# Kernel optimization log

Measured on AMD Instinct MI355X. Metric: run time of the kernel, lower is better.

The kernel has to match this reference:

```python
import jax, jax.numpy as jnp
import numpy as np

B, S, D, H = 4, 2048, 1024, 16
DK = D // H


def setup_inputs() -> dict:
    key = jax.random.key(0)
    ks = jax.random.split(key, 11)
    std = 1.0 / np.sqrt(D)
    mk = lambda k: jax.random.uniform(k, (D, D), jnp.float32, -std, std)
    mb = lambda k: jax.random.uniform(k, (D,), jnp.float32, -std, std)
    return {
        "query": jax.random.normal(ks[0], (B, S, D), jnp.float32),
        "key": jax.random.normal(ks[1], (B, S, D), jnp.float32),
        "value": jax.random.normal(ks[2], (B, S, D), jnp.float32),
        "Wq": mk(ks[3]), "bq": mb(ks[4]),
        "Wk": mk(ks[5]), "bk": mb(ks[6]),
        "Wv": mk(ks[7]), "bv": mb(ks[8]),
        "Wo": mk(ks[9]), "bo": mb(ks[10]),
    }


def reference(query, key, value, Wq, bq, Wk, bk, Wv, bv, Wo, bo):
    # Linear projections (torch Linear: x @ W.T + b)
    Q = query @ Wq.T + bq   # [B,S,D]
    K = key @ Wk.T + bk
    V = value @ Wv.T + bv
    # split heads -> [B,H,S,DK]
    Q = Q.reshape(B, S, H, DK).transpose(0, 2, 1, 3)
    K = K.reshape(B, S, H, DK).transpose(0, 2, 1, 3)
    V = V.reshape(B, S, H, DK).transpose(0, 2, 1, 3)
    scale = 1.0 / jnp.sqrt(jnp.asarray(DK, Q.dtype))
    scores = jnp.einsum("bhqd,bhkd->bhqk", Q, K) * scale  # [B,H,S,S]
    attn = jax.nn.softmax(scores, axis=-1)
    out = jnp.einsum("bhqk,bhkd->bhqd", attn, V)          # [B,H,S,DK]
    out = out.transpose(0, 2, 1, 3).reshape(B, S, D)       # [B,S,D]
    return out @ Wo.T + bo
```

## Files before the change

### kernel.cpp

```cpp
#include <hip/hip_runtime.h>
#include <hip/hip_bf16.h>
#include <stdint.h>


using f32x4  = __attribute__((ext_vector_type(4))) float;
using f32x16 = __attribute__((ext_vector_type(16))) float;
using s16x8  = __attribute__((ext_vector_type(8))) short;
using u16x8  = __attribute__((ext_vector_type(8))) unsigned short;
using u16x4  = __attribute__((ext_vector_type(4))) unsigned short;

#define MFMA16(a, b, c) __builtin_amdgcn_mfma_f32_16x16x32_bf16((a), (b), (c), 0, 0, 0)
#define MFMA32(a, b, c) __builtin_amdgcn_mfma_f32_32x32x16_bf16((a), (b), (c), 0, 0, 0)

#define GLL16(gptr, lptr)                                                      \
  __builtin_amdgcn_global_load_lds(                                            \
      (const __attribute__((address_space(1))) void*)(gptr),                   \
      (__attribute__((address_space(3))) void*)(lptr), 16, 0, 0)

__device__ __forceinline__ unsigned short f2bf(float f) {
  union { __hip_bfloat16 h; unsigned short u; } cv;
  cv.h = __float2bfloat16(f);
  return cv.u;
}

__device__ __forceinline__ unsigned int pkbf(float a, float b) {
  return (unsigned int)f2bf(a) | ((unsigned int)f2bf(b) << 16);
}

__device__ __forceinline__ s16x8 pack8(const float4& a, const float4& b) {
  union { u16x8 u; s16x8 s; } cv;
  cv.u[0] = f2bf(a.x); cv.u[1] = f2bf(a.y); cv.u[2] = f2bf(a.z); cv.u[3] = f2bf(a.w);
  cv.u[4] = f2bf(b.x); cv.u[5] = f2bf(b.y); cv.u[6] = f2bf(b.z); cv.u[7] = f2bf(b.w);
  return cv.s;
}

__global__ __launch_bounds__(256) void cast_w_kernel(
    const float* __restrict__ wq, const float* __restrict__ wk,
    const float* __restrict__ wv, const float* __restrict__ wo,
    unsigned short* __restrict__ dst) {
  int i = blockIdx.x * 256 + threadIdx.x;
  int m = i >> 18;
  int off = i & 0x3FFFF;
  const float* src = (m == 0) ? wq : (m == 1) ? wk : (m == 2) ? wv : wo;
  float4 v = reinterpret_cast<const float4*>(src)[off];
  u16x4 o;
  o[0] = f2bf(v.x); o[1] = f2bf(v.y); o[2] = f2bf(v.z); o[3] = f2bf(v.w);
  *reinterpret_cast<u16x4*>(dst + (size_t)i * 4) = o;
}

__global__ __launch_bounds__(256) void gemm_qkv_kernel(
    const float* __restrict__ xq, const float* __restrict__ xk, const float* __restrict__ xv,
    const unsigned short* __restrict__ wbf,
    const float* __restrict__ bq, const float* __restrict__ bk, const float* __restrict__ bv,
    unsigned short* __restrict__ Qh, unsigned short* __restrict__ Kh,
    unsigned short* __restrict__ Vh) {
  const int z = blockIdx.z;
  const float* X = (z == 0) ? xq : (z == 1) ? xk : xv;
  const float* bias = (z == 0) ? bq : (z == 1) ? bk : bv;
  const unsigned short* W = wbf + (size_t)z * 1048576;
  unsigned short* dst = (z == 0) ? Qh : (z == 1) ? Kh : Vh;
  const float qscale = (z == 0) ? 0.18033688011112042f : 1.0f;

  __shared__ __align__(16) float Af[128 * 32];
  __shared__ __align__(16) unsigned short Bs[128 * 32];

  const int t = threadIdx.x;
  const int lane = t & 63, w = t >> 6;
  const int g = lane >> 4, c = lane & 15;
  const int wm = (w >> 1) * 64, wn = (w & 1) * 64;
  const int n0 = (blockIdx.y & 7) * 128;
  const int m0 = (blockIdx.x * 8 + (blockIdx.y >> 3)) * 128;

  f32x4 acc[4][4];
#pragma unroll
  for (int i = 0; i < 4; i++)
#pragma unroll
    for (int j = 0; j < 4; j++) acc[i][j] = (f32x4)0.0f;

  const int ar = lane >> 3;
  const int acs = (lane & 7) ^ ar;
  const int br_ = lane >> 2;
  const int bcs = (lane & 3) ^ (br_ & 3);

  for (int k0 = 0; k0 < 1024; k0 += 32) {
    __syncthreads();
#pragma unroll
    for (int i = 0; i < 4; i++) {
      int ii = w * 4 + i;
      const float* gsrc = X + (size_t)(m0 + ii * 8 + ar) * 1024 + k0 + acs * 4;
      GLL16(gsrc, &Af[ii * 256]);
    }
#pragma unroll
    for (int i = 0; i < 2; i++) {
      int ii = w * 2 + i;
      const unsigned short* gsrc = W + (size_t)(n0 + ii * 16 + br_) * 1024 + k0 + bcs * 8;
      GLL16(gsrc, &Bs[ii * 512]);
    }
    __syncthreads();

    s16x8 af[4], bfr[4];
#pragma unroll
    for (int mt = 0; mt < 4; mt++) {
      int r = wm + mt * 16 + c;
      int x = r & 7;
      const float* rowp = &Af[r * 32];
      float4 f0 = *reinterpret_cast<const float4*>(rowp + (((g * 2) ^ x) << 2));
      float4 f1 = *reinterpret_cast<const float4*>(rowp + (((g * 2 + 1) ^ x) << 2));
      af[mt] = pack8(f0, f1);
    }
#pragma unroll
    for (int nt = 0; nt < 4; nt++) {
      int r = wn + nt * 16 + c;
      bfr[nt] = *reinterpret_cast<const s16x8*>(&Bs[r * 32 + ((g ^ (r & 3)) << 3)]);
    }
#pragma unroll
    for (int mt = 0; mt < 4; mt++)
#pragma unroll
      for (int nt = 0; nt < 4; nt++)
        acc[mt][nt] = MFMA16(af[mt], bfr[nt], acc[mt][nt]);
  }

#pragma unroll
  for (int mt = 0; mt < 4; mt++)
#pragma unroll
    for (int nt = 0; nt < 4; nt++) {
      int n = n0 + wn + nt * 16 + c;
      float bb = bias[n];
      int h = n >> 6, dk = n & 63;
#pragma unroll
      for (int r = 0; r < 4; r++) {
        int m = m0 + wm + mt * 16 + g * 4 + r;
        int b = m >> 11, s = m & 2047;
        dst[(((size_t)b * 16 + h) * 2048 + s) * 64 + dk] =
            f2bf((acc[mt][nt][r] + bb) * qscale);
      }
    }
}

__global__ __launch_bounds__(256) void gemm_out_kernel(
    const unsigned short* __restrict__ AO, const unsigned short* __restrict__ Wo,
    const float* __restrict__ bo, float* __restrict__ out) {
  __shared__ __align__(16) unsigned short Asm_[128 * 32];
  __shared__ __align__(16) unsigned short Bsm_[128 * 32];

  const int t = threadIdx.x;
  const int lane = t & 63, w = t >> 6;
  const int g = lane >> 4, c = lane & 15;
  const int wm = (w >> 1) * 64, wn = (w & 1) * 64;
  const int n0 = (blockIdx.y & 7) * 128;
  const int m0 = (blockIdx.x * 8 + (blockIdx.y >> 3)) * 128;

  f32x4 acc[4][4];
#pragma unroll
  for (int i = 0; i < 4; i++)
#pragma unroll
    for (int j = 0; j < 4; j++) acc[i][j] = (f32x4)0.0f;

  const int br_ = lane >> 2;
  const int bcs = (lane & 3) ^ (br_ & 3);

  for (int k0 = 0; k0 < 1024; k0 += 32) {
    __syncthreads();
#pragma unroll
    for (int i = 0; i < 2; i++) {
      int ii = w * 2 + i;
      const unsigned short* ga = AO + (size_t)(m0 + ii * 16 + br_) * 1024 + k0 + bcs * 8;
      GLL16(ga, &Asm_[ii * 512]);
      const unsigned short* gb = Wo + (size_t)(n0 + ii * 16 + br_) * 1024 + k0 + bcs * 8;
      GLL16(gb, &Bsm_[ii * 512]);
    }
    __syncthreads();

    s16x8 af[4], bfr[4];
#pragma unroll
    for (int mt = 0; mt < 4; mt++) {
      int r = wm + mt * 16 + c;
      af[mt] = *reinterpret_cast<const s16x8*>(&Asm_[r * 32 + ((g ^ (r & 3)) << 3)]);
    }
#pragma unroll
    for (int nt = 0; nt < 4; nt++) {
      int r = wn + nt * 16 + c;
      bfr[nt] = *reinterpret_cast<const s16x8*>(&Bsm_[r * 32 + ((g ^ (r & 3)) << 3)]);
    }
#pragma unroll
    for (int mt = 0; mt < 4; mt++)
#pragma unroll
      for (int nt = 0; nt < 4; nt++)
        acc[mt][nt] = MFMA16(af[mt], bfr[nt], acc[mt][nt]);
  }

#pragma unroll
  for (int mt = 0; mt < 4; mt++)
#pragma unroll
    for (int nt = 0; nt < 4; nt++) {
      int n = n0 + wn + nt * 16 + c;
      float bb = bo[n];
#pragma unroll
      for (int r = 0; r < 4; r++) {
        int m = m0 + wm + mt * 16 + g * 4 + r;
        out[(size_t)m * 1024 + n] = acc[mt][nt][r] + bb;
      }
    }
}

__global__ __launch_bounds__(512) void attn_kernel(
    const unsigned short* __restrict__ Qh, const unsigned short* __restrict__ Kh,
    const unsigned short* __restrict__ Vh, unsigned short* __restrict__ AO) {
  const int bh = blockIdx.x * 8 + (blockIdx.y >> 3);
  const int b = bh >> 4, h = bh & 15;
  const int q0 = (blockIdx.y & 7) * 256;
  const int t = threadIdx.x, lane = t & 63, w = t >> 6;
  const int lo = lane & 31, hi = lane >> 5;

  __shared__ __align__(16) unsigned short Ks[2][64 * 64];
  __shared__ __align__(16) unsigned short Vt[2][64 * 64];

  const size_t kvbase = (size_t)bh * 2048 * 64;

  s16x8 qb[4];
  {
    const unsigned short* qp = Qh + kvbase + (size_t)(q0 + w * 32 + lo) * 64;
#pragma unroll
    for (int ks = 0; ks < 4; ks++)
      qb[ks] = *reinterpret_cast<const s16x8*>(qp + ks * 16 + hi * 8);
  }

  f32x16 oacc[2];
  oacc[0] = (f32x16)0.0f; oacc[1] = (f32x16)0.0f;
  float lsum = 0.0f;

  const int skrow = t >> 3, sks = t & 7;
  const int kgc = sks ^ (skrow & 7);
  const int vkrow = t >> 3, vd0 = (t & 7) * 8;

  uint4 kk, vv;
  kk = *reinterpret_cast<const uint4*>(Kh + kvbase + (size_t)skrow * 64 + kgc * 8);
  vv = *reinterpret_cast<const uint4*>(Vh + kvbase + (size_t)vkrow * 64 + vd0);
  *reinterpret_cast<uint4*>(&Ks[0][(size_t)t * 8]) = kk;
  {
    const unsigned short* vs = reinterpret_cast<const unsigned short*>(&vv);
#pragma unroll
    for (int j = 0; j < 8; j++)
      Vt[0][(vd0 + j) * 64 + (((vkrow >> 3) ^ j) << 3) + (vkrow & 7)] = vs[j];
  }

  for (int it = 0; it < 32; ++it) {
    const int cur = it & 1, nxt = cur ^ 1;
    const bool more = (it < 31);
    if (more) {
      const int kv = (it + 1) * 64;
      kk = *reinterpret_cast<const uint4*>(Kh + kvbase + (size_t)(kv + skrow) * 64 + kgc * 8);
      vv = *reinterpret_cast<const uint4*>(Vh + kvbase + (size_t)(kv + vkrow) * 64 + vd0);
    }
    __syncthreads();

    f32x16 st[2];
    st[0] = (f32x16)0.0f; st[1] = (f32x16)0.0f;
#pragma unroll
    for (int kb = 0; kb < 2; kb++)
#pragma unroll
      for (int ks = 0; ks < 4; ks++) {
        s16x8 ka = *reinterpret_cast<const s16x8*>(
            &Ks[cur][(kb * 32 + lo) * 64 + (((ks * 2 + hi) ^ (lo & 7)) << 3)]);
        st[kb] = MFMA32(ka, qb[ks], st[kb]);
      }

    s16x8 pa[4];
    float part = 0.0f;
#pragma unroll
    for (int kb = 0; kb < 2; kb++) {
      float e[16];
#pragma unroll
      for (int r = 0; r < 16; r++) { e[r] = exp2f(st[kb][r]); part += e[r]; }
#pragma unroll
      for (int half = 0; half < 2; half++) {
        const float* eb = e + half * 8;
        unsigned int x1 = pkbf(eb[0], eb[1]);
        unsigned int x2 = pkbf(eb[2], eb[3]);
        unsigned int y1 = pkbf(eb[4], eb[5]);
        unsigned int y2 = pkbf(eb[6], eb[7]);
        asm volatile("v_permlane32_swap_b32 %0, %1" : "+v"(x1), "+v"(y1));
        asm volatile("v_permlane32_swap_b32 %0, %1" : "+v"(x2), "+v"(y2));
        uint4 u;
        u.x = x1; u.y = x2; u.z = y1; u.w = y2;
        pa[kb * 2 + half] = *reinterpret_cast<const s16x8*>(&u);
      }
    }
    lsum += part;

    if (more) {
      *reinterpret_cast<uint4*>(&Ks[nxt][(size_t)t * 8]) = kk;
      const unsigned short* vs = reinterpret_cast<const unsigned short*>(&vv);
#pragma unroll
      for (int j = 0; j < 8; j++)
        Vt[nxt][(vd0 + j) * 64 + (((vkrow >> 3) ^ j) << 3) + (vkrow & 7)] = vs[j];
    }

#pragma unroll
    for (int ks = 0; ks < 4; ks++)
#pragma unroll
      for (int db = 0; db < 2; db++) {
        s16x8 vb = *reinterpret_cast<const s16x8*>(
            &Vt[cur][(db * 32 + lo) * 64 + (((ks * 2 + hi) ^ (lo & 7)) << 3)]);
        oacc[db] = MFMA32(pa[ks], vb, oacc[db]);
      }
  }

  float ltot = lsum + __shfl_xor(lsum, 32);
  float linv = 1.0f / ltot;
#pragma unroll
  for (int r = 0; r < 16; r++) {
    int qr = (r & 3) + ((r >> 2) << 3) + (hi << 2);
    float inv_r = __shfl(linv, qr);
    int srow = q0 + w * 32 + qr;
    size_t obase = ((size_t)b * 2048 + srow) * 1024 + (size_t)h * 64;
    AO[obase + lo]      = f2bf(oacc[0][r] * inv_r);
    AO[obase + 32 + lo] = f2bf(oacc[1][r] * inv_r);
  }
}

extern "C" void kernel_launch(void* const* d_in, const int* in_sizes, int n_in,
                              void* d_out, int out_size, void* d_ws, size_t ws_size,
                              hipStream_t stream) {
  const float* query = (const float*)d_in[0];
  const float* key   = (const float*)d_in[1];
  const float* value = (const float*)d_in[2];
  const float* Wq = (const float*)d_in[3];
  const float* bq = (const float*)d_in[4];
  const float* Wk = (const float*)d_in[5];
  const float* bk = (const float*)d_in[6];
  const float* Wv = (const float*)d_in[7];
  const float* bv = (const float*)d_in[8];
  const float* Wo = (const float*)d_in[9];
  const float* bo = (const float*)d_in[10];

  uint8_t* wsb = (uint8_t*)d_ws;
  unsigned short* wbf = (unsigned short*)wsb;
  unsigned short* Qh  = (unsigned short*)(wsb + 8388608);
  unsigned short* Kh  = (unsigned short*)(wsb + 8388608 + 16777216);
  unsigned short* Vh  = (unsigned short*)(wsb + 8388608 + 2 * 16777216);
  unsigned short* AO  = (unsigned short*)(wsb + 8388608 + 3 * 16777216);

  cast_w_kernel<<<dim3(4096), dim3(256), 0, stream>>>(Wq, Wk, Wv, Wo, wbf);
  gemm_qkv_kernel<<<dim3(8, 64, 3), dim3(256), 0, stream>>>(
      query, key, value, wbf, bq, bk, bv, Qh, Kh, Vh);
  attn_kernel<<<dim3(8, 64), dim3(512), 0, stream>>>(Qh, Kh, Vh, AO);
  gemm_out_kernel<<<dim3(8, 64), dim3(256), 0, stream>>>(
      AO, wbf + (size_t)3 * 1048576, bo, (float*)d_out);
}
```

Before: 234.8 us.

## Tune attention inner loop: fast exp2, bitwise bf16 pack, setprio, V-store skew

Swaps exp2f for the hardware exp2 builtin and replaces the bf16 conversion with a manual round-to-nearest-even bit trick, in both the softmax and the pack8 helper. Wraps the MFMA blocks in s_setprio so matrix work gets issue priority over other waves. Rotates the per-thread order of the V-transpose LDS stores to reduce bank conflicts, and splits the exponent sum into four partial accumulators to shorten the dependency chain. The bit-trick rounding does not handle NaN and the builtin exp2 skips denormal handling, which is acceptable for softmax inputs.

```diff
diff --git a/kernel.cpp b/kernel.cpp
--- a/kernel.cpp
+++ b/kernel.cpp
@@ -23,15 +23,23 @@
   return cv.u;
 }
 
-__device__ __forceinline__ unsigned int pkbf(float a, float b) {
-  return (unsigned int)f2bf(a) | ((unsigned int)f2bf(b) << 16);
+__device__ __forceinline__ unsigned int pkrne(float a, float b) {
+  unsigned int ua = __builtin_bit_cast(unsigned int, a);
+  unsigned int ub = __builtin_bit_cast(unsigned int, b);
+  ua = ua + 0x7FFFu + ((ua >> 16) & 1u);
+  ub = ub + 0x7FFFu + ((ub >> 16) & 1u);
+  return (ua >> 16) | (ub & 0xFFFF0000u);
+}
+
+__device__ __forceinline__ float exp2a(float x) {
+  return __builtin_amdgcn_exp2f(x);
 }
 
 __device__ __forceinline__ s16x8 pack8(const float4& a, const float4& b) {
-  union { u16x8 u; s16x8 s; } cv;
-  cv.u[0] = f2bf(a.x); cv.u[1] = f2bf(a.y); cv.u[2] = f2bf(a.z); cv.u[3] = f2bf(a.w);
-  cv.u[4] = f2bf(b.x); cv.u[5] = f2bf(b.y); cv.u[6] = f2bf(b.z); cv.u[7] = f2bf(b.w);
-  return cv.s;
+  uint4 u;
+  u.x = pkrne(a.x, a.y); u.y = pkrne(a.z, a.w);
+  u.z = pkrne(b.x, b.y); u.w = pkrne(b.z, b.w);
+  return *reinterpret_cast<const s16x8*>(&u);
 }
 
 __global__ __launch_bounds__(256) void cast_w_kernel(
@@ -232,6 +240,7 @@
   const int skrow = t >> 3, sks = t & 7;
   const int kgc = sks ^ (skrow & 7);
   const int vkrow = t >> 3, vd0 = (t & 7) * 8;
+  const int vx = t & 7;
 
   uint4 kk, vv;
   kk = *reinterpret_cast<const uint4*>(Kh + kvbase + (size_t)skrow * 64 + kgc * 8);
@@ -240,8 +249,10 @@
   {
     const unsigned short* vs = reinterpret_cast<const unsigned short*>(&vv);
 #pragma unroll
-    for (int j = 0; j < 8; j++)
-      Vt[0][(vd0 + j) * 64 + (((vkrow >> 3) ^ j) << 3) + (vkrow & 7)] = vs[j];
+    for (int j = 0; j < 8; j++) {
+      int e = j ^ vx;
+      Vt[0][(vd0 + e) * 64 + (((vkrow >> 3) ^ e) << 3) + (vkrow & 7)] = vs[e];
+    }
   }
 
   for (int it = 0; it < 32; ++it) {
@@ -256,6 +267,7 @@
 
     f32x16 st[2];
     st[0] = (f32x16)0.0f; st[1] = (f32x16)0.0f;
+    __builtin_amdgcn_s_setprio(1);
 #pragma unroll
     for (int kb = 0; kb < 2; kb++)
 #pragma unroll
@@ -264,21 +276,28 @@
             &Ks[cur][(kb * 32 + lo) * 64 + (((ks * 2 + hi) ^ (lo & 7)) << 3)]);
         st[kb] = MFMA32(ka, qb[ks], st[kb]);
       }
+    __builtin_amdgcn_s_setprio(0);
 
     s16x8 pa[4];
-    float part = 0.0f;
+    float s0 = 0.0f, s1 = 0.0f, s2 = 0.0f, s3 = 0.0f;
 #pragma unroll
     for (int kb = 0; kb < 2; kb++) {
       float e[16];
 #pragma unroll
-      for (int r = 0; r < 16; r++) { e[r] = exp2f(st[kb][r]); part += e[r]; }
+      for (int r = 0; r < 16; r += 4) {
+        e[r]     = exp2a(st[kb][r]);
+        e[r + 1] = exp2a(st[kb][r + 1]);
+        e[r + 2] = exp2a(st[kb][r + 2]);
+        e[r + 3] = exp2a(st[kb][r + 3]);
+        s0 += e[r]; s1 += e[r + 1]; s2 += e[r + 2]; s3 += e[r + 3];
+      }
 #pragma unroll
       for (int half = 0; half < 2; half++) {
         const float* eb = e + half * 8;
-        unsigned int x1 = pkbf(eb[0], eb[1]);
-        unsigned int x2 = pkbf(eb[2], eb[3]);
-        unsigned int y1 = pkbf(eb[4], eb[5]);
-        unsigned int y2 = pkbf(eb[6], eb[7]);
+        unsigned int x1 = pkrne(eb[0], eb[1]);
+        unsigned int x2 = pkrne(eb[2], eb[3]);
+        unsigned int y1 = pkrne(eb[4], eb[5]);
+        unsigned int y2 = pkrne(eb[6], eb[7]);
         asm volatile("v_permlane32_swap_b32 %0, %1" : "+v"(x1), "+v"(y1));
         asm volatile("v_permlane32_swap_b32 %0, %1" : "+v"(x2), "+v"(y2));
         uint4 u;
@@ -286,16 +305,19 @@
         pa[kb * 2 + half] = *reinterpret_cast<const s16x8*>(&u);
       }
     }
-    lsum += part;
+    lsum += (s0 + s1) + (s2 + s3);
 
     if (more) {
       *reinterpret_cast<uint4*>(&Ks[nxt][(size_t)t * 8]) = kk;
       const unsigned short* vs = reinterpret_cast<const unsigned short*>(&vv);
 #pragma unroll
-      for (int j = 0; j < 8; j++)
-        Vt[nxt][(vd0 + j) * 64 + (((vkrow >> 3) ^ j) << 3) + (vkrow & 7)] = vs[j];
-    }
-
+      for (int j = 0; j < 8; j++) {
+        int e = j ^ vx;
+        Vt[nxt][(vd0 + e) * 64 + (((vkrow >> 3) ^ e) << 3) + (vkrow & 7)] = vs[e];
+      }
+    }
+
+    __builtin_amdgcn_s_setprio(1);
 #pragma unroll
     for (int ks = 0; ks < 4; ks++)
 #pragma unroll
@@ -304,6 +326,7 @@
             &Vt[cur][(db * 32 + lo) * 64 + (((ks * 2 + hi) ^ (lo & 7)) << 3)]);
         oacc[db] = MFMA32(pa[ks], vb, oacc[db]);
       }
+    __builtin_amdgcn_s_setprio(0);
   }
 
   float ltot = lsum + __shfl_xor(lsum, 32);
```

Result: slower. 281.4 us (+19.8%).
